# Kernel tuning notes

Hardware: AMD Instinct MI355X
Metric: run time of the kernel (lower is better)

The kernel has to match this reference:

```python
import jax, jax.numpy as jnp
import numpy as np

NUM_FEAT = 1024
NUM_GROUP = 16
DIM_K = NUM_FEAT // NUM_GROUP  # 64
FEAT_DIM = 64
WAVE_LENGTH = 1000.0


def position_embedding(box, ctx_box):
    # box: (M,4), ctx_box: (N,4) corner encoding -> (M*N, 64)
    xmin, ymin, xmax, ymax = jnp.split(box, 4, axis=1)            # (M,1) each
    bw = xmax - xmin + 1.0
    bh = ymax - ymin + 1.0
    cx = 0.5 * (xmin + xmax)
    cy = 0.5 * (ymin + ymax)
    cxmin, cymin, cxmax, cymax = jnp.split(ctx_box, 4, axis=1)    # (N,1) each
    cbw = cxmax - cxmin + 1.0
    cbh = cymax - cymin + 1.0
    ccx = 0.5 * (cxmin + cxmax)
    ccy = 0.5 * (cymin + cymax)
    dx = jnp.log(jnp.clip(jnp.abs((cx - ccx.T) / bw), 1e-3))      # (M,N)
    dy = jnp.log(jnp.clip(jnp.abs((cy - ccy.T) / bh), 1e-3))
    dw = jnp.log(cbw.T / bw)
    dh = jnp.log(cbh.T / bh)
    pos = jnp.stack((dx, dy, dw, dh), axis=2)                     # (M,N,4)
    feat_range = jnp.arange(FEAT_DIM // 8, dtype=jnp.float32)     # (8,)
    dim_mat = jnp.power(jnp.float32(WAVE_LENGTH), (8.0 / FEAT_DIM) * feat_range)
    div = (100.0 * pos)[..., None] / dim_mat                      # (M,N,4,8)
    emb = jnp.concatenate((jnp.sin(div), jnp.cos(div)), axis=3)   # (M,N,4,16)
    M, N = pos.shape[0], pos.shape[1]
    return emb.reshape(M * N, FEAT_DIM)


def setup_inputs() -> dict:
    key = jax.random.key(0)
    ks = jax.random.split(key, 12)
    M, N = 512, 1024

    def make_boxes(k, n):
        k1, k2 = jax.random.split(k)
        xy = jax.random.uniform(k1, (n, 2), dtype=jnp.float32) * 800.0
        wh = jax.random.uniform(k2, (n, 2), dtype=jnp.float32) * 200.0 + 1.0
        return jnp.concatenate([xy, xy + wh], axis=1)             # valid corners

    return {
        "feat": jax.random.normal(ks[0], (M, NUM_FEAT), dtype=jnp.float32),
        "ctx_feat": jax.random.normal(ks[1], (N, NUM_FEAT), dtype=jnp.float32),
        "box": make_boxes(ks[2], M),
        "ctx_box": make_boxes(ks[3], N),
        # torch Linear stores weight as (out, in); apply as x @ W.T + b
        "w_fc_gt": jax.random.normal(ks[4], (NUM_FEAT, 1024), dtype=jnp.float32) * 0.01,
        "b_fc_gt": jnp.zeros((NUM_FEAT,), dtype=jnp.float32),
        "w_fc_ctx": jax.random.normal(ks[5], (NUM_FEAT, 1024), dtype=jnp.float32) * 0.01,
        "b_fc_ctx": jnp.zeros((NUM_FEAT,), dtype=jnp.float32),
        "w_pos_gt": jax.random.normal(ks[6], (NUM_GROUP, FEAT_DIM), dtype=jnp.float32) * 0.01,
        "b_pos_gt": jnp.zeros((NUM_GROUP,), dtype=jnp.float32),
        "w_pos_ctx": jax.random.normal(ks[7], (NUM_GROUP, FEAT_DIM), dtype=jnp.float32) * 0.01,
        "b_pos_ctx": jnp.zeros((NUM_GROUP,), dtype=jnp.float32),
        # grouped 1x1 conv (16384 -> 1024, groups=16): per-group weight (64 out, 1024 in)
        "w_conv": jax.random.normal(ks[8], (NUM_GROUP, DIM_K, NUM_FEAT), dtype=jnp.float32) * 0.02,
        "b_conv": jnp.zeros((NUM_FEAT,), dtype=jnp.float32),
    }


def reference(feat, ctx_feat, box, ctx_box,
              w_fc_gt, b_fc_gt, w_fc_ctx, b_fc_ctx,
              w_pos_gt, b_pos_gt, w_pos_ctx, b_pos_ctx,
              w_conv, b_conv):
    M, N = feat.shape[0], ctx_feat.shape[0]
    # positional bias per group: (M*N,64) -relu-> linear -> (G,M,N)
    pe_gt = jax.nn.relu(position_embedding(box, ctx_box))
    pos_gt = (pe_gt @ w_pos_gt.T + b_pos_gt).T.reshape(NUM_GROUP, M, N)
    pe_ctx = jax.nn.relu(position_embedding(ctx_box, box))
    pos_ctx = (pe_ctx @ w_pos_ctx.T + b_pos_ctx).T.reshape(NUM_GROUP, N, M)
    # grouped projections
    q = (feat @ w_fc_gt.T + b_fc_gt).reshape(M, NUM_GROUP, DIM_K)
    k = (ctx_feat @ w_fc_ctx.T + b_fc_ctx).reshape(N, NUM_GROUP, DIM_K)
    scores = jnp.einsum('mgd,ngd->gmn', q, k) / np.float32(np.sqrt(DIM_K))  # (G,M,N)
    # gt <- ctx attention with log-position bias
    w1 = jax.nn.softmax(jnp.log(jnp.clip(pos_gt, 1e-6)) + scores, axis=-1)  # (G,M,N)
    att1 = jnp.einsum('gmn,nc->mgc', w1, ctx_feat)                          # (M,G,1024)
    out_gt = jnp.einsum('mgc,goc->mgo', att1, w_conv).reshape(M, NUM_FEAT) + b_conv
    # ctx <- gt attention (note: original module reuses gt_ctx_linear_out here)
    w2 = jax.nn.softmax(jnp.log(jnp.clip(pos_ctx, 1e-6)) + scores.transpose(0, 2, 1), axis=-1)  # (G,N,M)
    att2 = jnp.einsum('gnm,mc->ngc', w2, feat)                              # (N,G,1024)
    out_ctx = jnp.einsum('ngc,goc->ngo', att2, w_conv).reshape(N, NUM_FEAT) + b_conv
    return out_gt, out_ctx
```

## Files before the change

kernel.cpp:

```cpp
#include <hip/hip_runtime.h>
#include <math.h>


typedef __attribute__((ext_vector_type(8))) short short8;
typedef __attribute__((ext_vector_type(4))) float floatx4;
typedef __attribute__((ext_vector_type(4))) _Float16 half4;

__device__ inline unsigned short f32_bf16_rne(float x) {
    union { float f; unsigned u; } v; v.f = x;
    unsigned u = v.u;
    return (unsigned short)((u + 0x7fffu + ((u >> 16) & 1u)) >> 16);
}

__device__ inline float bf16_f32(unsigned short h) {
    union { unsigned u; float f; } v; v.u = (unsigned)h << 16;
    return v.f;
}

__device__ __forceinline__ floatx4 mfma16(short8 a, short8 b, floatx4 c) {
    return __builtin_amdgcn_mfma_f32_16x16x32_bf16(a, b, c, 0, 0, 0);
}

__device__ __forceinline__ void gemm_tile_bf16(
    const unsigned short* __restrict__ Ab, int lda,
    const unsigned short* __restrict__ Bb, int ldb, int K,
    unsigned short* __restrict__ Cb, int ldc,
    const float* __restrict__ biasvec,
    unsigned short* As, unsigned short* Bs)
{
    const int tid = threadIdx.x;
    const int lr = tid >> 2;
    const int lk = (tid & 3) * 8;
    const int lane = tid & 63;
    const int wave = tid >> 6;
    const int qr = (wave >> 1) * 32;
    const int qc = (wave & 1) * 32;
    const int m = lane & 15;
    const int quad = lane >> 4;

    const unsigned short* Ap = Ab + (long long)lr * lda + lk;
    const unsigned short* Bp = Bb + (long long)lr * ldb + lk;
    unsigned short* AsW = As + lr * 72 + lk;
    unsigned short* BsW = Bs + lr * 72 + lk;
    const unsigned short* a0p = As + (qr + m) * 72 + quad * 8;
    const unsigned short* b0p = Bs + (qc + m) * 72 + quad * 8;

    floatx4 acc00 = {0.f,0.f,0.f,0.f}, acc01 = {0.f,0.f,0.f,0.f};
    floatx4 acc10 = {0.f,0.f,0.f,0.f}, acc11 = {0.f,0.f,0.f,0.f};

    int4 pa0 = *(const int4*)Ap;
    int4 pa1 = *(const int4*)(Ap + 32);
    int4 pb0 = *(const int4*)Bp;
    int4 pb1 = *(const int4*)(Bp + 32);
    int4 qa0 = *(const int4*)(Ap + 64);
    int4 qa1 = *(const int4*)(Ap + 96);
    int4 qb0 = *(const int4*)(Bp + 64);
    int4 qb1 = *(const int4*)(Bp + 96);

    for (int k0 = 0; ; ) {
        __syncthreads();
        *(int4*)AsW        = pa0;
        *(int4*)(AsW + 32) = pa1;
        *(int4*)BsW        = pb0;
        *(int4*)(BsW + 32) = pb1;
        __syncthreads();
        pa0 = qa0; pa1 = qa1; pb0 = qb0; pb1 = qb1;
        const int kf = k0 + 128;
        if (kf < K) {
            qa0 = *(const int4*)(Ap + kf);
            qa1 = *(const int4*)(Ap + kf + 32);
            qb0 = *(const int4*)(Bp + kf);
            qb1 = *(const int4*)(Bp + kf + 32);
        }
        #pragma unroll
        for (int kk = 0; kk < 64; kk += 32) {
            short8 a0 = *(const short8*)(a0p + kk);
            short8 a1 = *(const short8*)(a0p + 16 * 72 + kk);
            short8 b0 = *(const short8*)(b0p + kk);
            short8 b1 = *(const short8*)(b0p + 16 * 72 + kk);
            acc00 = mfma16(a0, b0, acc00);
            acc01 = mfma16(a0, b1, acc01);
            acc10 = mfma16(a1, b0, acc10);
            acc11 = mfma16(a1, b1, acc11);
        }
        k0 += 64;
        if (k0 >= K) break;
    }

    float bias0 = 0.f, bias1 = 0.f;
    if (biasvec) { bias0 = biasvec[qc + m]; bias1 = biasvec[qc + 16 + m]; }

    const floatx4 accs[2][2] = { {acc00, acc01}, {acc10, acc11} };
    #pragma unroll
    for (int i = 0; i < 2; ++i)
        #pragma unroll
        for (int r = 0; r < 4; ++r) {
            const int lrow = qr + i * 16 + quad * 4 + r;
            #pragma unroll
            for (int j = 0; j < 2; ++j) {
                const int lcol = qc + j * 16 + m;
                float val = accs[i][j][r] + (j ? bias1 : bias0);
                Cb[(long long)lrow * ldc + lcol] = f32_bf16_rne(val);
            }
        }
}

__global__ __launch_bounds__(256) void projvt_kernel(
    const unsigned short* __restrict__ in_bf, const unsigned short* __restrict__ wgt,
    const unsigned short* __restrict__ wctx,
    const float* __restrict__ bgt, const float* __restrict__ bctx,
    unsigned short* __restrict__ qk,
    const unsigned short* __restrict__ wconv, unsigned short* __restrict__ vt)
{
    __shared__ __align__(16) unsigned short As[64 * 72];
    __shared__ __align__(16) unsigned short Bs[64 * 72];
    if (blockIdx.z == 0) {
        const int bm = blockIdx.x * 64, bn = blockIdx.y * 64;
        const unsigned short* B = (bm < 512) ? wgt : wctx;
        const float* bias = (bm < 512) ? bgt : bctx;
        gemm_tile_bf16(in_bf + (long long)bm * 1024, 1024,
                       B + (long long)bn * 1024, 1024, 1024,
                       qk + (long long)bm * 1024 + bn, 1024,
                       bias + bn, As, Bs);
    } else {
        const int g = blockIdx.y;
        const int bn = blockIdx.x * 64;
        gemm_tile_bf16(wconv + (long long)g * 65536, 1024,
                       in_bf + (long long)bn * 1024, 1024, 1024,
                       vt + (long long)g * 98304 + bn, 1536,
                       nullptr, As, Bs);
    }
}

__global__ __launch_bounds__(256) void pos_bias_kernel(
    const float* __restrict__ box, const float* __restrict__ ctx_box,
    const float* __restrict__ w_gt, const float* __restrict__ b_gt,
    const float* __restrict__ w_ctx, const float* __restrict__ b_ctx,
    _Float16* __restrict__ bias_gt, _Float16* __restrict__ bias_ctx)
{
    const bool first = (blockIdx.z == 0);
    const float* boxA = first ? box : ctx_box;
    const float* boxB = first ? ctx_box : box;
    const float* w_pos = first ? w_gt : w_ctx;
    const float* b_pos = first ? b_gt : b_ctx;
    _Float16* out = first ? bias_gt : bias_ctx;
    const int shift = first ? 10 : 9;

    __shared__ __align__(16) unsigned short AsH[64 * 72];
    __shared__ __align__(16) unsigned short AsL[64 * 72];
    __shared__ __align__(16) unsigned short BsH[16 * 72];
    __shared__ __align__(16) unsigned short BsL[16 * 72];

    const int tid = threadIdx.x;

    {
        const int g = tid >> 4;
        const int d = (tid & 15) * 4;
        float4 wv = *(const float4*)(w_pos + g * 64 + d);
        ushort4 h, l;
        h.x = f32_bf16_rne(wv.x); l.x = f32_bf16_rne(wv.x - bf16_f32(h.x));
        h.y = f32_bf16_rne(wv.y); l.y = f32_bf16_rne(wv.y - bf16_f32(h.y));
        h.z = f32_bf16_rne(wv.z); l.z = f32_bf16_rne(wv.z - bf16_f32(h.z));
        h.w = f32_bf16_rne(wv.w); l.w = f32_bf16_rne(wv.w - bf16_f32(h.w));
        *(ushort4*)&BsH[g * 72 + d] = h;
        *(ushort4*)&BsL[g * 72 + d] = l;
    }

    const long long pbase = (long long)blockIdx.x * 64;
    {
        const int pl = tid & 63;
        const int p = tid >> 6;
        const long long pair = pbase + pl;
        const int i = (int)(pair >> shift);
        const int j = (int)(pair & ((1 << shift) - 1));
        float4 ba = *(const float4*)(boxA + i * 4);
        float4 bb = *(const float4*)(boxB + j * 4);
        float posv;
        if (p == 0) {
            float bw = ba.z - ba.x + 1.f;
            float cx = 0.5f * (ba.x + ba.z), ccx = 0.5f * (bb.x + bb.z);
            posv = __logf(fmaxf(fabsf((cx - ccx) / bw), 1e-3f));
        } else if (p == 1) {
            float bh = ba.w - ba.y + 1.f;
            float cy = 0.5f * (ba.y + ba.w), ccy = 0.5f * (bb.y + bb.w);
            posv = __logf(fmaxf(fabsf((cy - ccy) / bh), 1e-3f));
        } else if (p == 2) {
            float bw = ba.z - ba.x + 1.f, cbw = bb.z - bb.x + 1.f;
            posv = __logf(cbw / bw);
        } else {
            float bh = ba.w - ba.y + 1.f, cbh = bb.w - bb.y + 1.f;
            posv = __logf(cbh / bh);
        }
        const float w100[8] = {100.f, 42.169650342f, 17.782794100f, 7.498942093f,
                               3.162277660f, 1.333521432f, 0.562341325f, 0.237137371f};
        short8 sh, sl, ch, cl;
        #pragma unroll
        for (int f = 0; f < 8; ++f) {
            float s, c;
            __sincosf(posv * w100[f], &s, &c);
            s = fmaxf(s, 0.f);
            c = fmaxf(c, 0.f);
            unsigned short hs = f32_bf16_rne(s);
            unsigned short hc = f32_bf16_rne(c);
            sh[f] = (short)hs; sl[f] = (short)f32_bf16_rne(s - bf16_f32(hs));
            ch[f] = (short)hc; cl[f] = (short)f32_bf16_rne(c - bf16_f32(hc));
        }
        *(short8*)&AsH[pl * 72 + p * 16]     = sh;
        *(short8*)&AsH[pl * 72 + p * 16 + 8] = ch;
        *(short8*)&AsL[pl * 72 + p * 16]     = sl;
        *(short8*)&AsL[pl * 72 + p * 16 + 8] = cl;
    }
    __syncthreads();

    const int lane = tid & 63;
    const int w = tid >> 6;
    const int m = lane & 15;
    const int quad = lane >> 4;
    const unsigned short* apH = &AsH[(w * 16 + m) * 72 + quad * 8];
    const unsigned short* apL = &AsL[(w * 16 + m) * 72 + quad * 8];
    const unsigned short* bpH = &BsH[m * 72 + quad * 8];
    const unsigned short* bpL = &BsL[m * 72 + quad * 8];
    floatx4 acc = {0.f, 0.f, 0.f, 0.f};
    acc = mfma16(*(const short8*)apH,        *(const short8*)bpH,        acc);
    acc = mfma16(*(const short8*)(apH + 32), *(const short8*)(bpH + 32), acc);
    acc = mfma16(*(const short8*)apH,        *(const short8*)bpL,        acc);
    acc = mfma16(*(const short8*)(apH + 32), *(const short8*)(bpL + 32), acc);
    acc = mfma16(*(const short8*)apL,        *(const short8*)bpH,        acc);
    acc = mfma16(*(const short8*)(apL + 32), *(const short8*)(bpH + 32), acc);

    const float bpv = b_pos[m];
    half4 o;
    #pragma unroll
    for (int r = 0; r < 4; ++r)
        o[r] = (_Float16)__logf(fmaxf(acc[r] + bpv, 1e-6f));
    *(half4*)(out + (long long)m * 524288 + pbase + w * 16 + quad * 4) = o;
}

template <int NC>
__device__ __forceinline__ void attn_body(
    int g, int bx,
    const unsigned short* __restrict__ qA, const unsigned short* __restrict__ qB,
    const _Float16* __restrict__ bias, const unsigned short* __restrict__ vt,
    int vt_colbase, const float* __restrict__ b_conv, float* __restrict__ outp,
    unsigned short* wpack, float* redA, float* redB)
{
    constexpr int NCOL = NC * 64;
    constexpr int WS = NCOL + 8;
    constexpr int SHIFT = (NC == 16) ? 10 : 9;

    const int bm = bx * 16;
    const int tid = threadIdx.x;
    const int lane = tid & 63;
    const int w = tid >> 6;
    const int m = lane & 15;
    const int quad = lane >> 4;

    _Float16* bb = (_Float16*)wpack;
    {
        const _Float16* bsrc = bias + (long long)g * 524288 + (long long)bm * NCOL;
        #pragma unroll
        for (int i = 0; i < (16 * NCOL) / (256 * 8); ++i) {
            const int idx = (i * 256 + tid) * 8;
            const int row = idx >> SHIFT;
            const int col = idx & (NCOL - 1);
            *(int4*)(bb + row * WS + col) = *(const int4*)(bsrc + idx);
        }
    }

    const unsigned short* ap = qA + (long long)(bm + m) * 1024 + g * 64 + quad * 8;
    short8 aq0 = *(const short8*)ap;
    short8 aq1 = *(const short8*)(ap + 32);

    const unsigned short* bbase = qB + (long long)(w * 16 + m) * 1024 + g * 64 + quad * 8;
    short8 b0 = *(const short8*)bbase;
    short8 b1 = *(const short8*)(bbase + 32);

    __syncthreads();

    const _Float16* brow = bb + (quad * 4) * WS + w * 16 + m;

    float v[NC][4];
    #pragma unroll
    for (int c = 0; c < NC; ++c) {
        short8 nb0, nb1;
        if (c + 1 < NC) {
            const unsigned short* nb = bbase + (long long)(c + 1) * 65536;
            nb0 = *(const short8*)nb;
            nb1 = *(const short8*)(nb + 32);
        }
        float bv[4];
        #pragma unroll
        for (int r = 0; r < 4; ++r)
            bv[r] = (float)brow[r * WS + c * 64];
        floatx4 acc = {0.f, 0.f, 0.f, 0.f};
        acc = mfma16(aq0, b0, acc);
        acc = mfma16(aq1, b1, acc);
        #pragma unroll
        for (int r = 0; r < 4; ++r)
            v[c][r] = fmaf(0.125f, acc[r], bv[r]);
        b0 = nb0; b1 = nb1;
    }

    float rmax[4];
    #pragma unroll
    for (int r = 0; r < 4; ++r) {
        float mx = v[0][r];
        #pragma unroll
        for (int c = 1; c < NC; ++c) mx = fmaxf(mx, v[c][r]);
        #pragma unroll
        for (int off = 1; off < 16; off <<= 1)
            mx = fmaxf(mx, __shfl_xor(mx, off, 64));
        rmax[r] = mx;
    }
    if (m == 0) {
        #pragma unroll
        for (int r = 0; r < 4; ++r) redA[w * 16 + quad * 4 + r] = rmax[r];
    }
    __syncthreads();
    #pragma unroll
    for (int r = 0; r < 4; ++r)
        rmax[r] = fmaxf(fmaxf(redA[quad*4+r], redA[16 + quad*4+r]),
                        fmaxf(redA[32 + quad*4+r], redA[48 + quad*4+r]));

    float rsum[4] = {0.f, 0.f, 0.f, 0.f};
    #pragma unroll
    for (int c = 0; c < NC; ++c)
        #pragma unroll
        for (int r = 0; r < 4; ++r) {
            v[c][r] = __expf(v[c][r] - rmax[r]);
            rsum[r] += v[c][r];
        }
    #pragma unroll
    for (int r = 0; r < 4; ++r)
        #pragma unroll
        for (int off = 1; off < 16; off <<= 1)
            rsum[r] += __shfl_xor(rsum[r], off, 64);
    if (m == 0) {
        #pragma unroll
        for (int r = 0; r < 4; ++r) redB[w * 16 + quad * 4 + r] = rsum[r];
    }
    __syncthreads();
    float rinv[4];
    #pragma unroll
    for (int r = 0; r < 4; ++r)
        rinv[r] = 1.f / (redB[quad*4+r] + redB[16 + quad*4+r] +
                         redB[32 + quad*4+r] + redB[48 + quad*4+r]);

    #pragma unroll
    for (int c = 0; c < NC; ++c)
        #pragma unroll
        for (int r = 0; r < 4; ++r)
            wpack[(quad * 4 + r) * WS + c * 64 + w * 16 + m] =
                f32_bf16_rne(v[c][r] * rinv[r]);

    const unsigned short* vbase = vt + (long long)g * 98304
                                + (long long)(w * 16 + m) * 1536 + vt_colbase + quad * 8;
    short8 vb0 = *(const short8*)vbase;
    short8 vb1 = *(const short8*)(vbase + 32);

    __syncthreads();

    floatx4 oacc = {0.f, 0.f, 0.f, 0.f};
    const unsigned short* awp = wpack + m * WS + quad * 8;
    #pragma unroll
    for (int kc = 0; kc < NC; ++kc) {
        short8 nv0, nv1;
        if (kc + 1 < NC) {
            const unsigned short* nv = vbase + (kc + 1) * 64;
            nv0 = *(const short8*)nv;
            nv1 = *(const short8*)(nv + 32);
        }
        short8 a0 = *(const short8*)(awp + kc * 64);
        short8 a1 = *(const short8*)(awp + kc * 64 + 32);
        oacc = mfma16(a0, vb0, oacc);
        oacc = mfma16(a1, vb1, oacc);
        vb0 = nv0; vb1 = nv1;
    }

    const int o = w * 16 + m;
    const float bc = b_conv[g * 64 + o];
    #pragma unroll
    for (int r = 0; r < 4; ++r)
        outp[(long long)(bm + quad * 4 + r) * 1024 + g * 64 + o] = oacc[r] + bc;
}

__global__ __launch_bounds__(256) void attn_out_kernel(
    const unsigned short* __restrict__ qk,
    const _Float16* __restrict__ bias_gt, const _Float16* __restrict__ bias_ctx,
    const unsigned short* __restrict__ vt, const float* __restrict__ b_conv,
    float* __restrict__ out_gt, float* __restrict__ out_ctx)
{
    __shared__ __align__(16) unsigned short wpack[16 * 1032];
    __shared__ float redA[64], redB[64];

    const int bx = blockIdx.x;
    if (bx < 512) {
        attn_body<16>(bx >> 5, bx & 31, qk, qk + 524288LL, bias_gt, vt, 512,
                      b_conv, out_gt, wpack, redA, redB);
    } else {
        const int b2 = bx - 512;
        attn_body<8>(b2 >> 6, b2 & 63, qk + 524288LL, qk, bias_ctx, vt, 0,
                     b_conv, out_ctx, wpack, redA, redB);
    }
}

__global__ __launch_bounds__(256) void conv5_f32_bf16(
    const float* s0, unsigned short* d0, int n0,
    const float* s1, unsigned short* d1, int n1,
    const float* s2, unsigned short* d2, int n2,
    const float* s3, unsigned short* d3, int n3,
    const float* s4, unsigned short* d4, int n4)
{
    const float* s; unsigned short* d; int n;
    switch (blockIdx.y) {
        case 0: s = s0; d = d0; n = n0; break;
        case 1: s = s1; d = d1; n = n1; break;
        case 2: s = s2; d = d2; n = n2; break;
        case 3: s = s3; d = d3; n = n3; break;
        default: s = s4; d = d4; n = n4; break;
    }
    int idx = (blockIdx.x * 256 + threadIdx.x) * 4;
    if (idx < n) {
        float4 v = *(const float4*)(s + idx);
        ushort4 o;
        o.x = f32_bf16_rne(v.x); o.y = f32_bf16_rne(v.y);
        o.z = f32_bf16_rne(v.z); o.w = f32_bf16_rne(v.w);
        *(ushort4*)(d + idx) = o;
    }
}

extern "C" void kernel_launch(void* const* d_in, const int* in_sizes, int n_in,
                              void* d_out, int out_size, void* d_ws, size_t ws_size,
                              hipStream_t stream)
{
    const float* feat     = (const float*)d_in[0];
    const float* ctx_feat = (const float*)d_in[1];
    const float* box      = (const float*)d_in[2];
    const float* ctx_box  = (const float*)d_in[3];
    const float* w_fc_gt  = (const float*)d_in[4];
    const float* b_fc_gt  = (const float*)d_in[5];
    const float* w_fc_ctx = (const float*)d_in[6];
    const float* b_fc_ctx = (const float*)d_in[7];
    const float* w_pos_gt = (const float*)d_in[8];
    const float* b_pos_gt = (const float*)d_in[9];
    const float* w_pos_ctx= (const float*)d_in[10];
    const float* b_pos_ctx= (const float*)d_in[11];
    const float* w_conv   = (const float*)d_in[12];
    const float* b_conv   = (const float*)d_in[13];

    float* ws = (float*)d_ws;
    unsigned short* in_bf   = (unsigned short*)ws;
    unsigned short* ctx_bf  = in_bf + 524288LL;
    unsigned short* qk_bf   = in_bf + 1572864LL;
    _Float16* bias_gt  = (_Float16*)(ws + 1572864LL);
    _Float16* bias_ctx = (_Float16*)(ws + 5767168LL);
    unsigned short* wconv_bf = (unsigned short*)(ws + 9961472LL);
    unsigned short* vt_bf    = (unsigned short*)(ws + 10485760LL);
    unsigned short* wfcgt_bf = (unsigned short*)(ws + 11272192LL);
    unsigned short* wfcctx_bf= wfcgt_bf + 1048576LL;

    float* out_gt  = (float*)d_out;
    float* out_ctx = (float*)d_out + 524288LL;

    hipLaunchKernelGGL(conv5_f32_bf16, dim3(1024, 5), dim3(256), 0, stream,
                       feat, in_bf, 524288,
                       ctx_feat, ctx_bf, 1048576,
                       w_fc_gt, wfcgt_bf, 1048576,
                       w_fc_ctx, wfcctx_bf, 1048576,
                       w_conv, wconv_bf, 1048576);

    hipLaunchKernelGGL(pos_bias_kernel, dim3(8192, 1, 2), dim3(256), 0, stream,
                       box, ctx_box, w_pos_gt, b_pos_gt, w_pos_ctx, b_pos_ctx,
                       bias_gt, bias_ctx);

    hipLaunchKernelGGL(projvt_kernel, dim3(24, 16, 2), dim3(256), 0, stream,
                       in_bf, wfcgt_bf, wfcctx_bf, b_fc_gt, b_fc_ctx, qk_bf,
                       wconv_bf, vt_bf);

    hipLaunchKernelGGL(attn_out_kernel, dim3(1536), dim3(256), 0, stream,
                       qk_bf, bias_gt, bias_ctx, vt_bf, b_conv, out_gt, out_ctx);
}
```

Baseline: 177.8 us.

## Pack Q/K/V tiles in MFMA fragment order and fuse prep kernels

The projection GEMMs now stage their output tiles through shared memory and write them in a packed layout that matches the MFMA fragment order. The attention kernel can then load Q, K and V operands as contiguous 16-byte per-lane reads, with a two-deep register prefetch, instead of strided row reads. The bf16 conversion kernel is merged into the position-bias kernel as extra blocks, which removes one launch. Both the position-bias and attention epilogues now stage through shared memory for coalesced vector stores. This adds extra barriers and shared-memory traffic, and the GEMM load mapping changes from a 4-thread to an 8-thread row split.

New measurement: 158.2 us. 11.0% less time.

```diff
diff --git a/kernel.cpp b/kernel.cpp
--- a/kernel.cpp
+++ b/kernel.cpp
@@ -21,16 +21,16 @@
     return __builtin_amdgcn_mfma_f32_16x16x32_bf16(a, b, c, 0, 0, 0);
 }
 
-__device__ __forceinline__ void gemm_tile_bf16(
+__device__ __forceinline__ void gemm_tile_pack(
     const unsigned short* __restrict__ Ab, int lda,
     const unsigned short* __restrict__ Bb, int ldb, int K,
-    unsigned short* __restrict__ Cb, int ldc,
+    unsigned short* __restrict__ out_base,
     const float* __restrict__ biasvec,
     unsigned short* As, unsigned short* Bs)
 {
     const int tid = threadIdx.x;
-    const int lr = tid >> 2;
-    const int lk = (tid & 3) * 8;
+    const int lr = tid >> 3;
+    const int lk = (tid & 7) * 8;
     const int lane = tid & 63;
     const int wave = tid >> 6;
     const int qr = (wave >> 1) * 32;
@@ -38,10 +38,14 @@
     const int m = lane & 15;
     const int quad = lane >> 4;
 
-    const unsigned short* Ap = Ab + (long long)lr * lda + lk;
-    const unsigned short* Bp = Bb + (long long)lr * ldb + lk;
-    unsigned short* AsW = As + lr * 72 + lk;
-    unsigned short* BsW = Bs + lr * 72 + lk;
+    const unsigned short* Ap  = Ab + (long long)lr * lda + lk;
+    const unsigned short* Ap2 = Ap + 32LL * lda;
+    const unsigned short* Bp  = Bb + (long long)lr * ldb + lk;
+    const unsigned short* Bp2 = Bp + 32LL * ldb;
+    unsigned short* AsW  = As + lr * 72 + lk;
+    unsigned short* AsW2 = As + (lr + 32) * 72 + lk;
+    unsigned short* BsW  = Bs + lr * 72 + lk;
+    unsigned short* BsW2 = Bs + (lr + 32) * 72 + lk;
     const unsigned short* a0p = As + (qr + m) * 72 + quad * 8;
     const unsigned short* b0p = Bs + (qc + m) * 72 + quad * 8;
 
@@ -49,28 +53,28 @@
     floatx4 acc10 = {0.f,0.f,0.f,0.f}, acc11 = {0.f,0.f,0.f,0.f};
 
     int4 pa0 = *(const int4*)Ap;
-    int4 pa1 = *(const int4*)(Ap + 32);
+    int4 pa1 = *(const int4*)Ap2;
     int4 pb0 = *(const int4*)Bp;
-    int4 pb1 = *(const int4*)(Bp + 32);
+    int4 pb1 = *(const int4*)Bp2;
     int4 qa0 = *(const int4*)(Ap + 64);
-    int4 qa1 = *(const int4*)(Ap + 96);
+    int4 qa1 = *(const int4*)(Ap2 + 64);
     int4 qb0 = *(const int4*)(Bp + 64);
-    int4 qb1 = *(const int4*)(Bp + 96);
+    int4 qb1 = *(const int4*)(Bp2 + 64);
 
     for (int k0 = 0; ; ) {
         __syncthreads();
-        *(int4*)AsW        = pa0;
-        *(int4*)(AsW + 32) = pa1;
-        *(int4*)BsW        = pb0;
-        *(int4*)(BsW + 32) = pb1;
+        *(int4*)AsW  = pa0;
+        *(int4*)AsW2 = pa1;
+        *(int4*)BsW  = pb0;
+        *(int4*)BsW2 = pb1;
         __syncthreads();
         pa0 = qa0; pa1 = qa1; pb0 = qb0; pb1 = qb1;
         const int kf = k0 + 128;
         if (kf < K) {
             qa0 = *(const int4*)(Ap + kf);
-            qa1 = *(const int4*)(Ap + kf + 32);
+            qa1 = *(const int4*)(Ap2 + kf);
             qb0 = *(const int4*)(Bp + kf);
-            qb1 = *(const int4*)(Bp + kf + 32);
+            qb1 = *(const int4*)(Bp2 + kf);
         }
         #pragma unroll
         for (int kk = 0; kk < 64; kk += 32) {
@@ -90,6 +94,7 @@
     float bias0 = 0.f, bias1 = 0.f;
     if (biasvec) { bias0 = biasvec[qc + m]; bias1 = biasvec[qc + 16 + m]; }
 
+    __syncthreads();
     const floatx4 accs[2][2] = { {acc00, acc01}, {acc10, acc11} };
     #pragma unroll
     for (int i = 0; i < 2; ++i)
@@ -100,45 +105,88 @@
             for (int j = 0; j < 2; ++j) {
                 const int lcol = qc + j * 16 + m;
                 float val = accs[i][j][r] + (j ? bias1 : bias0);
-                Cb[(long long)lrow * ldc + lcol] = f32_bf16_rne(val);
+                As[lrow * 72 + lcol] = f32_bf16_rne(val);
             }
         }
+    __syncthreads();
+    #pragma unroll
+    for (int h = 0; h < 2; ++h) {
+        const int f = h * 2048 + tid * 8;
+        const int lanep = (f >> 3) & 63;
+        const int part = (f >> 9) & 1;
+        const int ploc = f >> 10;
+        const int row = ploc * 16 + (lanep & 15);
+        const int col = part * 32 + ((lanep >> 4) << 3);
+        short8 v8 = *(const short8*)&As[row * 72 + col];
+        *(short8*)(out_base + f) = v8;
+    }
 }
 
 __global__ __launch_bounds__(256) void projvt_kernel(
     const unsigned short* __restrict__ in_bf, const unsigned short* __restrict__ wgt,
     const unsigned short* __restrict__ wctx,
     const float* __restrict__ bgt, const float* __restrict__ bctx,
-    unsigned short* __restrict__ qk,
-    const unsigned short* __restrict__ wconv, unsigned short* __restrict__ vt)
+    unsigned short* __restrict__ qk_pack,
+    const unsigned short* __restrict__ wconv, unsigned short* __restrict__ vt_pack)
 {
     __shared__ __align__(16) unsigned short As[64 * 72];
     __shared__ __align__(16) unsigned short Bs[64 * 72];
     if (blockIdx.z == 0) {
-        const int bm = blockIdx.x * 64, bn = blockIdx.y * 64;
+        const int bm = blockIdx.x * 64;
+        const int g = blockIdx.y;
         const unsigned short* B = (bm < 512) ? wgt : wctx;
         const float* bias = (bm < 512) ? bgt : bctx;
-        gemm_tile_bf16(in_bf + (long long)bm * 1024, 1024,
-                       B + (long long)bn * 1024, 1024, 1024,
-                       qk + (long long)bm * 1024 + bn, 1024,
-                       bias + bn, As, Bs);
+        gemm_tile_pack(in_bf + (long long)bm * 1024, 1024,
+                       B + (long long)g * 65536, 1024, 1024,
+                       qk_pack + ((long long)g * 96 + blockIdx.x * 4) * 1024,
+                       bias + g * 64, As, Bs);
     } else {
+        const int cc = blockIdx.x;
         const int g = blockIdx.y;
-        const int bn = blockIdx.x * 64;
-        gemm_tile_bf16(wconv + (long long)g * 65536, 1024,
-                       in_bf + (long long)bn * 1024, 1024, 1024,
-                       vt + (long long)g * 98304 + bn, 1536,
+        gemm_tile_pack(wconv + (long long)g * 65536, 1024,
+                       in_bf + (long long)cc * 65536, 1024, 1024,
+                       vt_pack + ((long long)g * 24 + cc) * 4096,
                        nullptr, As, Bs);
     }
 }
 
-__global__ __launch_bounds__(256) void pos_bias_kernel(
+__global__ __launch_bounds__(256) void prep_kernel(
     const float* __restrict__ box, const float* __restrict__ ctx_box,
     const float* __restrict__ w_gt, const float* __restrict__ b_gt,
     const float* __restrict__ w_ctx, const float* __restrict__ b_ctx,
-    _Float16* __restrict__ bias_gt, _Float16* __restrict__ bias_ctx)
+    _Float16* __restrict__ bias_gt, _Float16* __restrict__ bias_ctx,
+    const float* s0, unsigned short* d0, int n0,
+    const float* s1, unsigned short* d1, int n1,
+    const float* s2, unsigned short* d2, int n2,
+    const float* s3, unsigned short* d3, int n3,
+    const float* s4, unsigned short* d4, int n4)
 {
-    const bool first = (blockIdx.z == 0);
+    const int bx = blockIdx.x;
+    if (bx >= 16384) {
+        const int bc = bx - 16384;
+        const int which = bc >> 10;
+        const int xb = bc & 1023;
+        const float* s; unsigned short* d; int n;
+        switch (which) {
+            case 0: s = s0; d = d0; n = n0; break;
+            case 1: s = s1; d = d1; n = n1; break;
+            case 2: s = s2; d = d2; n = n2; break;
+            case 3: s = s3; d = d3; n = n3; break;
+            default: s = s4; d = d4; n = n4; break;
+        }
+        int idx = (xb * 256 + threadIdx.x) * 4;
+        if (idx < n) {
+            float4 v = *(const float4*)(s + idx);
+            ushort4 o;
+            o.x = f32_bf16_rne(v.x); o.y = f32_bf16_rne(v.y);
+            o.z = f32_bf16_rne(v.z); o.w = f32_bf16_rne(v.w);
+            *(ushort4*)(d + idx) = o;
+        }
+        return;
+    }
+
+    const bool first = (bx < 8192);
+    const long long blk = first ? bx : (bx - 8192);
     const float* boxA = first ? box : ctx_box;
     const float* boxB = first ? ctx_box : box;
     const float* w_pos = first ? w_gt : w_ctx;
@@ -150,6 +198,7 @@
     __shared__ __align__(16) unsigned short AsL[64 * 72];
     __shared__ __align__(16) unsigned short BsH[16 * 72];
     __shared__ __align__(16) unsigned short BsL[16 * 72];
+    __shared__ _Float16 stg[16 * 68];
 
     const int tid = threadIdx.x;
 
@@ -166,7 +215,7 @@
         *(ushort4*)&BsL[g * 72 + d] = l;
     }
 
-    const long long pbase = (long long)blockIdx.x * 64;
+    const long long pbase = blk * 64;
     {
         const int pl = tid & 63;
         const int p = tid >> 6;
@@ -229,19 +278,22 @@
     acc = mfma16(*(const short8*)(apL + 32), *(const short8*)(bpH + 32), acc);
 
     const float bpv = b_pos[m];
-    half4 o;
     #pragma unroll
     for (int r = 0; r < 4; ++r)
-        o[r] = (_Float16)__logf(fmaxf(acc[r] + bpv, 1e-6f));
-    *(half4*)(out + (long long)m * 524288 + pbase + w * 16 + quad * 4) = o;
+        stg[m * 68 + w * 16 + quad * 4 + r] = (_Float16)__logf(fmaxf(acc[r] + bpv, 1e-6f));
+    __syncthreads();
+    const int g2 = tid >> 4, c16 = tid & 15;
+    *(half4*)(out + (long long)g2 * 524288 + pbase + c16 * 4) =
+        *(const half4*)&stg[g2 * 68 + c16 * 4];
 }
 
 template <int NC>
 __device__ __forceinline__ void attn_body(
     int g, int bx,
-    const unsigned short* __restrict__ qA, const unsigned short* __restrict__ qB,
-    const _Float16* __restrict__ bias, const unsigned short* __restrict__ vt,
-    int vt_colbase, const float* __restrict__ b_conv, float* __restrict__ outp,
+    const unsigned short* __restrict__ qk, int pA, int pB0,
+    const _Float16* __restrict__ bias,
+    const unsigned short* __restrict__ vt, int cc0,
+    const float* __restrict__ b_conv, float* __restrict__ outp,
     unsigned short* wpack, float* redA, float* redB)
 {
     constexpr int NCOL = NC * 64;
@@ -267,13 +319,16 @@
         }
     }
 
-    const unsigned short* ap = qA + (long long)(bm + m) * 1024 + g * 64 + quad * 8;
-    short8 aq0 = *(const short8*)ap;
-    short8 aq1 = *(const short8*)(ap + 32);
-
-    const unsigned short* bbase = qB + (long long)(w * 16 + m) * 1024 + g * 64 + quad * 8;
-    short8 b0 = *(const short8*)bbase;
-    short8 b1 = *(const short8*)(bbase + 32);
+    const unsigned short* abase = qk + ((long long)(g * 96 + pA)) * 1024;
+    short8 aq0 = *(const short8*)(abase + lane * 8);
+    short8 aq1 = *(const short8*)(abase + 512 + lane * 8);
+
+    const unsigned short* bptr = qk + ((long long)(g * 96 + pB0 + w)) * 1024 + lane * 8;
+    short8 B0[2], B1[2];
+    B0[0] = *(const short8*)bptr;
+    B1[0] = *(const short8*)(bptr + 512);
+    B0[1] = *(const short8*)(bptr + 4096);
+    B1[1] = *(const short8*)(bptr + 4096 + 512);
 
     __syncthreads();
 
@@ -282,24 +337,30 @@
     float v[NC][4];
     #pragma unroll
     for (int c = 0; c < NC; ++c) {
-        short8 nb0, nb1;
-        if (c + 1 < NC) {
-            const unsigned short* nb = bbase + (long long)(c + 1) * 65536;
-            nb0 = *(const short8*)nb;
-            nb1 = *(const short8*)(nb + 32);
-        }
         float bv[4];
         #pragma unroll
         for (int r = 0; r < 4; ++r)
             bv[r] = (float)brow[r * WS + c * 64];
         floatx4 acc = {0.f, 0.f, 0.f, 0.f};
-        acc = mfma16(aq0, b0, acc);
-        acc = mfma16(aq1, b1, acc);
+        acc = mfma16(aq0, B0[c & 1], acc);
+        acc = mfma16(aq1, B1[c & 1], acc);
+        if (c + 2 < NC) {
+            const unsigned short* nb = bptr + (long long)(c + 2) * 4096;
+            B0[c & 1] = *(const short8*)nb;
+            B1[c & 1] = *(const short8*)(nb + 512);
+        }
         #pragma unroll
         for (int r = 0; r < 4; ++r)
             v[c][r] = fmaf(0.125f, acc[r], bv[r]);
-        b0 = nb0; b1 = nb1;
-    }
+    }
+
+    const unsigned short* vptr = vt + ((long long)(g * 24 + cc0)) * 4096
+                               + w * 1024 + lane * 8;
+    short8 V0[2], V1[2];
+    V0[0] = *(const short8*)vptr;
+    V1[0] = *(const short8*)(vptr + 512);
+    V0[1] = *(const short8*)(vptr + 4096);
+    V1[1] = *(const short8*)(vptr + 4096 + 512);
 
     float rmax[4];
     #pragma unroll
@@ -353,41 +414,40 @@
             wpack[(quad * 4 + r) * WS + c * 64 + w * 16 + m] =
                 f32_bf16_rne(v[c][r] * rinv[r]);
 
-    const unsigned short* vbase = vt + (long long)g * 98304
-                                + (long long)(w * 16 + m) * 1536 + vt_colbase + quad * 8;
-    short8 vb0 = *(const short8*)vbase;
-    short8 vb1 = *(const short8*)(vbase + 32);
-
     __syncthreads();
 
     floatx4 oacc = {0.f, 0.f, 0.f, 0.f};
     const unsigned short* awp = wpack + m * WS + quad * 8;
     #pragma unroll
     for (int kc = 0; kc < NC; ++kc) {
-        short8 nv0, nv1;
-        if (kc + 1 < NC) {
-            const unsigned short* nv = vbase + (kc + 1) * 64;
-            nv0 = *(const short8*)nv;
-            nv1 = *(const short8*)(nv + 32);
-        }
         short8 a0 = *(const short8*)(awp + kc * 64);
         short8 a1 = *(const short8*)(awp + kc * 64 + 32);
-        oacc = mfma16(a0, vb0, oacc);
-        oacc = mfma16(a1, vb1, oacc);
-        vb0 = nv0; vb1 = nv1;
+        oacc = mfma16(a0, V0[kc & 1], oacc);
+        oacc = mfma16(a1, V1[kc & 1], oacc);
+        if (kc + 2 < NC) {
+            const unsigned short* nv = vptr + (long long)(kc + 2) * 4096;
+            V0[kc & 1] = *(const short8*)nv;
+            V1[kc & 1] = *(const short8*)(nv + 512);
+        }
     }
 
     const int o = w * 16 + m;
     const float bc = b_conv[g * 64 + o];
+    __syncthreads();
+    float* ot = (float*)wpack;
     #pragma unroll
     for (int r = 0; r < 4; ++r)
-        outp[(long long)(bm + quad * 4 + r) * 1024 + g * 64 + o] = oacc[r] + bc;
+        ot[(quad * 4 + r) * 68 + o] = oacc[r] + bc;
+    __syncthreads();
+    const int orow = tid >> 4, oc4 = (tid & 15) * 4;
+    float4 ov = *(const float4*)&ot[orow * 68 + oc4];
+    *(float4*)(outp + (long long)(bm + orow) * 1024 + g * 64 + oc4) = ov;
 }
 
 __global__ __launch_bounds__(256) void attn_out_kernel(
-    const unsigned short* __restrict__ qk,
+    const unsigned short* __restrict__ qk_pack,
     const _Float16* __restrict__ bias_gt, const _Float16* __restrict__ bias_ctx,
-    const unsigned short* __restrict__ vt, const float* __restrict__ b_conv,
+    const unsigned short* __restrict__ vt_pack, const float* __restrict__ b_conv,
     float* __restrict__ out_gt, float* __restrict__ out_ctx)
 {
     __shared__ __align__(16) unsigned short wpack[16 * 1032];
@@ -395,37 +455,16 @@
 
     const int bx = blockIdx.x;
     if (bx < 512) {
-        attn_body<16>(bx >> 5, bx & 31, qk, qk + 524288LL, bias_gt, vt, 512,
-                      b_conv, out_gt, wpack, redA, redB);
+        const int rb = bx & 31;
+        attn_body<16>(bx >> 5, rb, qk_pack, rb, 32,
+                      bias_gt, vt_pack, 8, b_conv, out_gt,
+                      wpack, redA, redB);
     } else {
         const int b2 = bx - 512;
-        attn_body<8>(b2 >> 6, b2 & 63, qk + 524288LL, qk, bias_ctx, vt, 0,
-                     b_conv, out_ctx, wpack, redA, redB);
-    }
-}
-
-__global__ __launch_bounds__(256) void conv5_f32_bf16(
-    const float* s0, unsigned short* d0, int n0,
-    const float* s1, unsigned short* d1, int n1,
-    const float* s2, unsigned short* d2, int n2,
-    const float* s3, unsigned short* d3, int n3,
-    const float* s4, unsigned short* d4, int n4)
-{
-    const float* s; unsigned short* d; int n;
-    switch (blockIdx.y) {
-        case 0: s = s0; d = d0; n = n0; break;
-        case 1: s = s1; d = d1; n = n1; break;
-        case 2: s = s2; d = d2; n = n2; break;
-        case 3: s = s3; d = d3; n = n3; break;
-        default: s = s4; d = d4; n = n4; break;
-    }
-    int idx = (blockIdx.x * 256 + threadIdx.x) * 4;
-    if (idx < n) {
-        float4 v = *(const float4*)(s + idx);
-        ushort4 o;
-        o.x = f32_bf16_rne(v.x); o.y = f32_bf16_rne(v.y);
-        o.z = f32_bf16_rne(v.z); o.w = f32_bf16_rne(v.w);
-        *(ushort4*)(d + idx) = o;
+        const int rb = b2 & 63;
+        attn_body<8>(b2 >> 6, rb, qk_pack, 32 + rb, 0,
+                     bias_ctx, vt_pack, 0, b_conv, out_ctx,
+                     wpack, redA, redB);
     }
 }
 
@@ -451,32 +490,30 @@
     float* ws = (float*)d_ws;
     unsigned short* in_bf   = (unsigned short*)ws;
     unsigned short* ctx_bf  = in_bf + 524288LL;
-    unsigned short* qk_bf   = in_bf + 1572864LL;
+    unsigned short* qk_pack = in_bf + 1572864LL;
     _Float16* bias_gt  = (_Float16*)(ws + 1572864LL);
     _Float16* bias_ctx = (_Float16*)(ws + 5767168LL);
     unsigned short* wconv_bf = (unsigned short*)(ws + 9961472LL);
-    unsigned short* vt_bf    = (unsigned short*)(ws + 10485760LL);
+    unsigned short* vt_pack  = (unsigned short*)(ws + 10485760LL);
     unsigned short* wfcgt_bf = (unsigned short*)(ws + 11272192LL);
     unsigned short* wfcctx_bf= wfcgt_bf + 1048576LL;
 
     float* out_gt  = (float*)d_out;
     float* out_ctx = (float*)d_out + 524288LL;
 
-    hipLaunchKernelGGL(conv5_f32_bf16, dim3(1024, 5), dim3(256), 0, stream,
+    hipLaunchKernelGGL(prep_kernel, dim3(21504), dim3(256), 0, stream,
+                       box, ctx_box, w_pos_gt, b_pos_gt, w_pos_ctx, b_pos_ctx,
+                       bias_gt, bias_ctx,
                        feat, in_bf, 524288,
                        ctx_feat, ctx_bf, 1048576,
                        w_fc_gt, wfcgt_bf, 1048576,
                        w_fc_ctx, wfcctx_bf, 1048576,
                        w_conv, wconv_bf, 1048576);
 
-    hipLaunchKernelGGL(pos_bias_kernel, dim3(8192, 1, 2), dim3(256), 0, stream,
-                       box, ctx_box, w_pos_gt, b_pos_gt, w_pos_ctx, b_pos_ctx,
-                       bias_gt, bias_ctx);
-
     hipLaunchKernelGGL(projvt_kernel, dim3(24, 16, 2), dim3(256), 0, stream,
-                       in_bf, wfcgt_bf, wfcctx_bf, b_fc_gt, b_fc_ctx, qk_bf,
-                       wconv_bf, vt_bf);
+                       in_bf, wfcgt_bf, wfcctx_bf, b_fc_gt, b_fc_ctx, qk_pack,
+                       wconv_bf, vt_pack);
 
     hipLaunchKernelGGL(attn_out_kernel, dim3(1536), dim3(256), 0, stream,
-                       qk_bf, bias_gt, bias_ctx, vt_bf, b_conv, out_gt, out_ctx);
-}
+                       qk_pack, bias_gt, bias_ctx, vt_pack, b_conv, out_gt, out_ctx);
+}
```
